# Kernel tuning notes

Measured on AMD Instinct MI355X. Metric: run time of the kernel, lower is better.

Reference implementation:

```python
import jax, jax.numpy as jnp
import numpy as np

DIM = 768
HEADS = 12


def setup_inputs() -> dict:
    key = jax.random.key(0)
    ks = jax.random.split(key, 7)
    B, N, S, C = 4, 1024, 1024, DIM
    query = jax.random.normal(ks[0], (B, N, C), dtype=jnp.float32)
    attn_weight = jax.random.normal(ks[1], (B, HEADS, N, S), dtype=jnp.float32) * 0.1
    s = 1.0 / np.sqrt(C)
    Wq = jax.random.normal(ks[2], (C, C), dtype=jnp.float32) * s
    Wk = jax.random.normal(ks[3], (C, C), dtype=jnp.float32) * s
    Wv = jax.random.normal(ks[4], (C, C), dtype=jnp.float32) * s
    Wo = jax.random.normal(ks[5], (C, C), dtype=jnp.float32) * s
    bo = jnp.zeros((C,), dtype=jnp.float32)
    return {"query": query, "attn_weight": attn_weight, "Wq": Wq, "Wk": Wk, "Wv": Wv, "Wo": Wo, "bo": bo}


def reference(query, attn_weight, Wq, Wk, Wv, Wo, bo):
    B, N, C = query.shape
    H = HEADS
    d = C // H
    scale = d ** -0.5
    # self-attention: key = value = query
    def heads(x):  # [B,N,C] -> [B,H,N,d]
        return x.reshape(B, -1, H, d).transpose(0, 2, 1, 3)
    q = heads(query @ Wq.T)
    k = heads(query @ Wk.T)
    v = heads(query @ Wv.T)
    attn = jnp.einsum('bhnd,bhsd->bhns', q, k) * scale
    log_attn = jax.nn.log_softmax(attn, axis=-1)
    attn = jax.nn.softmax(attn_weight + log_attn, axis=-1)
    out = jnp.einsum('bhns,bhsd->bhnd', attn, v)
    out = out.transpose(0, 2, 1, 3).reshape(B, N, C)
    out = out @ Wo.T + bo
    return out
```

## Files before the change

kernel.cpp:

```cpp
#include <hip/hip_runtime.h>
#include <cstdint>
#include <cstddef>

typedef unsigned short u16;
typedef unsigned int u32;
typedef float f32x4 __attribute__((ext_vector_type(4)));
typedef short bf16x8 __attribute__((ext_vector_type(8)));


#define GLOAD_LDS16(g, l)                                                        \
  __builtin_amdgcn_global_load_lds(                                              \
      (const __attribute__((address_space(1))) void*)(g),                        \
      (__attribute__((address_space(3))) void*)(l), 16, 0, 0)

__device__ __forceinline__ u16 f2bf(float f) {
  u32 u = __float_as_uint(f);
  u32 r = ((u >> 16) & 1u) + 0x7fffu;
  return (u16)((u + r) >> 16);
}

__device__ __forceinline__ float redmax16(float v) {
  v = fmaxf(v, __shfl_xor(v, 8, 16));
  v = fmaxf(v, __shfl_xor(v, 4, 16));
  v = fmaxf(v, __shfl_xor(v, 2, 16));
  v = fmaxf(v, __shfl_xor(v, 1, 16));
  return v;
}
__device__ __forceinline__ float redsum16(float v) {
  v += __shfl_xor(v, 8, 16);
  v += __shfl_xor(v, 4, 16);
  v += __shfl_xor(v, 2, 16);
  v += __shfl_xor(v, 1, 16);
  return v;
}

__global__ __launch_bounds__(256) void cast_all(
    const float* __restrict__ q, const float* __restrict__ wq, const float* __restrict__ wk,
    const float* __restrict__ wv, const float* __restrict__ wo,
    u16* __restrict__ X, u16* __restrict__ Wqkv, u16* __restrict__ Wob) {
  int id = blockIdx.x * 256 + threadIdx.x;
  const float* src;
  u16* dst;
  if (id < 786432) {
    src = q + (size_t)id * 4;       dst = X + (size_t)id * 4;
  } else if (id < 933888) {
    int o = id - 786432;  src = wq + (size_t)o * 4; dst = Wqkv + (size_t)o * 4;
  } else if (id < 1081344) {
    int o = id - 933888;  src = wk + (size_t)o * 4; dst = Wqkv + 589824 + (size_t)o * 4;
  } else if (id < 1228800) {
    int o = id - 1081344; src = wv + (size_t)o * 4; dst = Wqkv + 1179648 + (size_t)o * 4;
  } else {
    int o = id - 1228800; src = wo + (size_t)o * 4; dst = Wob + (size_t)o * 4;
  }
  float4 v = *(const float4*)src;
  uint2 o2;
  o2.x = (u32)f2bf(v.x) | ((u32)f2bf(v.y) << 16);
  o2.y = (u32)f2bf(v.z) | ((u32)f2bf(v.w) << 16);
  *(uint2*)dst = o2;
}

template <int MODE>
__global__ __launch_bounds__(256) void gemm_bt(
    const u16* __restrict__ A, const u16* __restrict__ Bm,
    u16* __restrict__ Cq, float* __restrict__ Cf, const float* __restrict__ bias) {
  constexpr int K = 768;
  __shared__ u16 As[128 * 64];
  __shared__ u16 Bs[128 * 64];
  const int tid = threadIdx.x;
  const int w = tid >> 6, lane = tid & 63, quad = lane >> 4, l16 = lane & 15;
  const int m0 = blockIdx.y * 128, n0 = blockIdx.x * 128;
  const int wm = (w >> 1) * 64, wn = (w & 1) * 64;
  const int xr = (l16 & 7) << 3;

  f32x4 acc[4][4];
#pragma unroll
  for (int i = 0; i < 4; ++i)
#pragma unroll
    for (int j = 0; j < 4; ++j)
#pragma unroll
      for (int r = 0; r < 4; ++r) acc[i][j][r] = 0.f;

  for (int kt = 0; kt < K; kt += 64) {
#pragma unroll
    for (int t = 0; t < 4; ++t) {
      int id = (t * 4 + w) * 64 + lane;
      int row = id >> 3;
      int scol = ((id & 7) ^ (row & 7)) << 3;
      GLOAD_LDS16(A + (size_t)(m0 + row) * K + kt + scol, As + (t * 4 + w) * 512);
      GLOAD_LDS16(Bm + (size_t)(n0 + row) * K + kt + scol, Bs + (t * 4 + w) * 512);
    }
    __syncthreads();
#pragma unroll
    for (int kk = 0; kk < 2; ++kk) {
      bf16x8 af[4], bfr[4];
#pragma unroll
      for (int mi = 0; mi < 4; ++mi)
        af[mi] = *(const bf16x8*)(As + (wm + mi * 16 + l16) * 64 + ((kk * 32 + quad * 8) ^ xr));
#pragma unroll
      for (int ni = 0; ni < 4; ++ni)
        bfr[ni] = *(const bf16x8*)(Bs + (wn + ni * 16 + l16) * 64 + ((kk * 32 + quad * 8) ^ xr));
#pragma unroll
      for (int mi = 0; mi < 4; ++mi)
#pragma unroll
        for (int ni = 0; ni < 4; ++ni)
          acc[mi][ni] = __builtin_amdgcn_mfma_f32_16x16x32_bf16(af[mi], bfr[ni], acc[mi][ni], 0, 0, 0);
    }
    __syncthreads();
  }

#pragma unroll
  for (int ni = 0; ni < 4; ++ni) {
    int cb = n0 + wn + ni * 16;
#pragma unroll
    for (int mi = 0; mi < 4; ++mi) {
#pragma unroll
      for (int r = 0; r < 4; ++r) {
        int m = m0 + wm + mi * 16 + quad * 4 + r;
        float v = acc[mi][ni][r];
        if (MODE == 0) {
          int t = cb / 768;
          int c = cb - t * 768;
          int h = c >> 6, dd = (c & 63) + l16;
          int b = m >> 10, ntok = m & 1023;
          Cq[(size_t)((t * 4 + b) * 12 + h) * 65536 + (size_t)ntok * 64 + dd] = f2bf(v);
        } else {
          int n = cb + l16;
          Cf[(size_t)m * 768 + n] = v + bias[n];
        }
      }
    }
  }
}

__global__ __launch_bounds__(256) void transpose_v(const u16* __restrict__ QKV,
                                                   u16* __restrict__ Vt) {
  __shared__ u16 tsm[64 * 72];
  const int bh = blockIdx.y, n0 = blockIdx.x * 64;
  const u16* V = QKV + (size_t)(96 + bh) * 65536;
  const int tid = threadIdx.x;
  const int r = tid >> 2, ch = tid & 3;
  *(int4*)(tsm + r * 72 + ch * 16) = *(const int4*)(V + (size_t)(n0 + r) * 64 + ch * 16);
  *(int4*)(tsm + r * 72 + ch * 16 + 8) = *(const int4*)(V + (size_t)(n0 + r) * 64 + ch * 16 + 8);
  __syncthreads();
  const int dd = tid >> 2;
  alignas(16) u16 buf[16];
#pragma unroll
  for (int i = 0; i < 16; ++i) buf[i] = tsm[(ch * 16 + i) * 72 + dd];
  u16* dst = Vt + ((size_t)bh * 64 + dd) * 1024 + n0 + ch * 16;
  *(int4*)dst = *(int4*)buf;
  *(int4*)(dst + 8) = *((int4*)buf + 1);
}

__global__ __launch_bounds__(256, 3) void attn_kernel(
    const u16* __restrict__ QKV, const u16* __restrict__ Vt,
    const float* __restrict__ W, u16* __restrict__ Oa) {
  __shared__ u16 Ks2[2][64 * 64];
  __shared__ u16 Vs2[2][64 * 64];
  __shared__ u16 Ps[4][16 * 72];
  const int tid = threadIdx.x;
  const int w = tid >> 6, lane = tid & 63, quad = lane >> 4, l16 = lane & 15;
  const int bh = blockIdx.y, q0 = blockIdx.x * 64;
  const u16* Qh = QKV + (size_t)bh * 65536;
  const u16* Kh = QKV + (size_t)(48 + bh) * 65536;
  const u16* Vth = Vt + (size_t)bh * 65536;
  const float* Wp = W + (size_t)bh * 1048576 + (size_t)(q0 + w * 16 + quad * 4) * 1024 + l16;
  const int xr = (l16 & 7) << 3;

  bf16x8 aq0, aq1;
  {
    int qrow = q0 + w * 16 + l16;
    aq0 = *(const bf16x8*)(Qh + (size_t)qrow * 64 + quad * 8);
    aq1 = *(const bf16x8*)(Qh + (size_t)qrow * 64 + 32 + quad * 8);
  }

  const int sid0 = (0 * 4 + w) * 64 + lane;
  const int sid1 = (1 * 4 + w) * 64 + lane;
  const int r0 = sid0 >> 3, sl0 = ((sid0 & 7) ^ (r0 & 7)) << 3;
  const int r1 = sid1 >> 3, sl1 = ((sid1 & 7) ^ (r1 & 7)) << 3;

  GLOAD_LDS16(Kh + (size_t)r0 * 64 + sl0, &Ks2[0][(0 * 4 + w) * 512]);
  GLOAD_LDS16(Kh + (size_t)r1 * 64 + sl1, &Ks2[0][(1 * 4 + w) * 512]);
  GLOAD_LDS16(Vth + (size_t)r0 * 1024 + sl0, &Vs2[0][(0 * 4 + w) * 512]);
  GLOAD_LDS16(Vth + (size_t)r1 * 1024 + sl1, &Vs2[0][(1 * 4 + w) * 512]);
  float wc[4][4];
#pragma unroll
  for (int r = 0; r < 4; ++r)
#pragma unroll
    for (int j = 0; j < 4; ++j) wc[j][r] = Wp[(size_t)r * 1024 + j * 16];

  f32x4 o[4];
  float mrow[4], lrow[4];
#pragma unroll
  for (int j = 0; j < 4; ++j)
#pragma unroll
    for (int r = 0; r < 4; ++r) o[j][r] = 0.f;
#pragma unroll
  for (int r = 0; r < 4; ++r) { mrow[r] = -1e30f; lrow[r] = 0.f; }

  for (int st = 0; st < 16; ++st) {
    const int cur = st & 1;
    __syncthreads();

    float wn[4][4];
    if (st < 15) {
      const int sn = (st + 1) * 64;
      GLOAD_LDS16(Kh + (size_t)(sn + r0) * 64 + sl0, &Ks2[cur ^ 1][(0 * 4 + w) * 512]);
      GLOAD_LDS16(Kh + (size_t)(sn + r1) * 64 + sl1, &Ks2[cur ^ 1][(1 * 4 + w) * 512]);
      GLOAD_LDS16(Vth + (size_t)r0 * 1024 + sn + sl0, &Vs2[cur ^ 1][(0 * 4 + w) * 512]);
      GLOAD_LDS16(Vth + (size_t)r1 * 1024 + sn + sl1, &Vs2[cur ^ 1][(1 * 4 + w) * 512]);
#pragma unroll
      for (int r = 0; r < 4; ++r)
#pragma unroll
        for (int j = 0; j < 4; ++j) wn[j][r] = Wp[(size_t)r * 1024 + sn + j * 16];
    }

    const u16* Kb = Ks2[cur];
    const u16* Vb = Vs2[cur];

    f32x4 sf[4];
#pragma unroll
    for (int j = 0; j < 4; ++j) {
#pragma unroll
      for (int r = 0; r < 4; ++r) sf[j][r] = 0.f;
      bf16x8 bk0 = *(const bf16x8*)(Kb + (j * 16 + l16) * 64 + ((quad * 8) ^ xr));
      bf16x8 bk1 = *(const bf16x8*)(Kb + (j * 16 + l16) * 64 + ((32 + quad * 8) ^ xr));
      sf[j] = __builtin_amdgcn_mfma_f32_16x16x32_bf16(aq0, bk0, sf[j], 0, 0, 0);
      sf[j] = __builtin_amdgcn_mfma_f32_16x16x32_bf16(aq1, bk1, sf[j], 0, 0, 0);
    }
    float lg[4][4];
#pragma unroll
    for (int j = 0; j < 4; ++j)
#pragma unroll
      for (int r = 0; r < 4; ++r) lg[j][r] = sf[j][r] * 0.125f + wc[j][r];

    float ps[4][4];
#pragma unroll
    for (int r = 0; r < 4; ++r) {
      float nm = fmaxf(fmaxf(lg[0][r], lg[1][r]), fmaxf(lg[2][r], lg[3][r]));
      nm = redmax16(nm);
      nm = fmaxf(nm, mrow[r]);
      float al = __expf(mrow[r] - nm);
      mrow[r] = nm;
      float rs = 0.f;
#pragma unroll
      for (int j = 0; j < 4; ++j) {
        ps[j][r] = __expf(lg[j][r] - nm);
        rs += ps[j][r];
      }
      rs = redsum16(rs);
      lrow[r] = lrow[r] * al + rs;
#pragma unroll
      for (int jd = 0; jd < 4; ++jd) o[jd][r] *= al;
    }
    u16* Pw = Ps[w];
#pragma unroll
    for (int j = 0; j < 4; ++j)
#pragma unroll
      for (int r = 0; r < 4; ++r) Pw[(quad * 4 + r) * 72 + j * 16 + l16] = f2bf(ps[j][r]);
#pragma unroll
    for (int kk = 0; kk < 2; ++kk) {
      bf16x8 ap = *(const bf16x8*)(Pw + l16 * 72 + kk * 32 + quad * 8);
#pragma unroll
      for (int jd = 0; jd < 4; ++jd) {
        bf16x8 bv = *(const bf16x8*)(Vb + (jd * 16 + l16) * 64 + ((kk * 32 + quad * 8) ^ xr));
        o[jd] = __builtin_amdgcn_mfma_f32_16x16x32_bf16(ap, bv, o[jd], 0, 0, 0);
      }
    }
    if (st < 15) {
#pragma unroll
      for (int r = 0; r < 4; ++r)
#pragma unroll
        for (int j = 0; j < 4; ++j) wc[j][r] = wn[j][r];
    }
  }

  const int b = bh / 12, h = bh - (bh / 12) * 12;
#pragma unroll
  for (int jd = 0; jd < 4; ++jd)
#pragma unroll
    for (int r = 0; r < 4; ++r) {
      int row = b * 1024 + q0 + w * 16 + quad * 4 + r;
      int col = h * 64 + jd * 16 + l16;
      Oa[(size_t)row * 768 + col] = f2bf(o[jd][r] / lrow[r]);
    }
}

extern "C" void kernel_launch(void* const* d_in, const int* in_sizes, int n_in,
                              void* d_out, int out_size, void* d_ws, size_t ws_size,
                              hipStream_t stream) {
  const float* q  = (const float*)d_in[0];
  const float* aw = (const float*)d_in[1];
  const float* wq = (const float*)d_in[2];
  const float* wk = (const float*)d_in[3];
  const float* wv = (const float*)d_in[4];
  const float* wo = (const float*)d_in[5];
  const float* bo = (const float*)d_in[6];
  float* out = (float*)d_out;
  char* ws = (char*)d_ws;
  u16* X    = (u16*)(ws);
  u16* Wqkv = (u16*)(ws + 6291456);
  u16* Wob  = (u16*)(ws + 9830400);
  u16* QKV  = (u16*)(ws + 11010048);
  u16* Vt   = (u16*)(ws + 29884416);
  u16* Oa   = (u16*)(ws + 36175872);

  cast_all<<<5376, 256, 0, stream>>>(q, wq, wk, wv, wo, X, Wqkv, Wob);
  gemm_bt<0><<<dim3(18, 32), 256, 0, stream>>>(X, Wqkv, QKV, nullptr, nullptr);
  transpose_v<<<dim3(16, 48), 256, 0, stream>>>(QKV, Vt);
  attn_kernel<<<dim3(16, 48), 256, 0, stream>>>(QKV, Vt, aw, Oa);
  gemm_bt<1><<<dim3(6, 32), 256, 0, stream>>>(Oa, Wob, nullptr, out, bo);
}
```

Baseline: 369.7 us.

## Add 64-row output GEMM, raise attention occupancy, swizzle P buffer

Replaces the output projection GEMM with a 64x128-tile variant, launching twice as many blocks so more CUs stay busy on the small 4096x768 problem. The attention kernel's launch bound goes from 3 to 4 blocks per CU. Its P scratch buffer switches from padded rows to an XOR-swizzled 64-wide layout, which shrinks LDS use and avoids bank conflicts. The final normalization uses a reciprocal multiply instead of a division. The tighter register budget could cause spills, and the smaller GEMM tile reuses each loaded operand less.

```diff
diff --git a/kernel.cpp b/kernel.cpp
--- a/kernel.cpp
+++ b/kernel.cpp
@@ -132,6 +132,69 @@
   }
 }
 
+__global__ __launch_bounds__(256) void gemm_bt64(
+    const u16* __restrict__ A, const u16* __restrict__ Bm,
+    float* __restrict__ Cf, const float* __restrict__ bias) {
+  constexpr int K = 768;
+  __shared__ u16 As[64 * 64];
+  __shared__ u16 Bs[128 * 64];
+  const int tid = threadIdx.x;
+  const int w = tid >> 6, lane = tid & 63, quad = lane >> 4, l16 = lane & 15;
+  const int m0 = blockIdx.y * 64, n0 = blockIdx.x * 128;
+  const int wm = (w >> 1) * 32, wn = (w & 1) * 64;
+  const int xr = (l16 & 7) << 3;
+
+  f32x4 acc[2][4];
+#pragma unroll
+  for (int i = 0; i < 2; ++i)
+#pragma unroll
+    for (int j = 0; j < 4; ++j)
+#pragma unroll
+      for (int r = 0; r < 4; ++r) acc[i][j][r] = 0.f;
+
+  for (int kt = 0; kt < K; kt += 64) {
+#pragma unroll
+    for (int t = 0; t < 4; ++t) {
+      int id = (t * 4 + w) * 64 + lane;
+      int row = id >> 3, scol = ((id & 7) ^ (row & 7)) << 3;
+      GLOAD_LDS16(Bm + (size_t)(n0 + row) * K + kt + scol, Bs + (t * 4 + w) * 512);
+      if (t < 2) {
+        GLOAD_LDS16(A + (size_t)(m0 + row) * K + kt + scol, As + (t * 4 + w) * 512);
+      }
+    }
+    __syncthreads();
+#pragma unroll
+    for (int kk = 0; kk < 2; ++kk) {
+      bf16x8 af[2], bfr[4];
+#pragma unroll
+      for (int mi = 0; mi < 2; ++mi)
+        af[mi] = *(const bf16x8*)(As + (wm + mi * 16 + l16) * 64 + ((kk * 32 + quad * 8) ^ xr));
+#pragma unroll
+      for (int ni = 0; ni < 4; ++ni)
+        bfr[ni] = *(const bf16x8*)(Bs + (wn + ni * 16 + l16) * 64 + ((kk * 32 + quad * 8) ^ xr));
+#pragma unroll
+      for (int mi = 0; mi < 2; ++mi)
+#pragma unroll
+        for (int ni = 0; ni < 4; ++ni)
+          acc[mi][ni] = __builtin_amdgcn_mfma_f32_16x16x32_bf16(af[mi], bfr[ni], acc[mi][ni], 0, 0, 0);
+    }
+    __syncthreads();
+  }
+
+#pragma unroll
+  for (int ni = 0; ni < 4; ++ni) {
+    int n = n0 + wn + ni * 16 + l16;
+#pragma unroll
+    for (int mi = 0; mi < 2; ++mi) {
+#pragma unroll
+      for (int r = 0; r < 4; ++r) {
+        int m = m0 + wm + mi * 16 + quad * 4 + r;
+        Cf[(size_t)m * 768 + n] = acc[mi][ni][r] + bias[n];
+      }
+    }
+  }
+}
+
 __global__ __launch_bounds__(256) void transpose_v(const u16* __restrict__ QKV,
                                                    u16* __restrict__ Vt) {
   __shared__ u16 tsm[64 * 72];
@@ -151,12 +214,12 @@
   *(int4*)(dst + 8) = *((int4*)buf + 1);
 }
 
-__global__ __launch_bounds__(256, 3) void attn_kernel(
+__global__ __launch_bounds__(256, 4) void attn_kernel(
     const u16* __restrict__ QKV, const u16* __restrict__ Vt,
     const float* __restrict__ W, u16* __restrict__ Oa) {
   __shared__ u16 Ks2[2][64 * 64];
   __shared__ u16 Vs2[2][64 * 64];
-  __shared__ u16 Ps[4][16 * 72];
+  __shared__ u16 Ps[4][16 * 64];
   const int tid = threadIdx.x;
   const int w = tid >> 6, lane = tid & 63, quad = lane >> 4, l16 = lane & 15;
   const int bh = blockIdx.y, q0 = blockIdx.x * 64;
@@ -256,10 +319,13 @@
 #pragma unroll
     for (int j = 0; j < 4; ++j)
 #pragma unroll
-      for (int r = 0; r < 4; ++r) Pw[(quad * 4 + r) * 72 + j * 16 + l16] = f2bf(ps[j][r]);
+      for (int r = 0; r < 4; ++r) {
+        int prow = quad * 4 + r;
+        Pw[prow * 64 + ((j * 16 + l16) ^ ((prow & 7) << 3))] = f2bf(ps[j][r]);
+      }
 #pragma unroll
     for (int kk = 0; kk < 2; ++kk) {
-      bf16x8 ap = *(const bf16x8*)(Pw + l16 * 72 + kk * 32 + quad * 8);
+      bf16x8 ap = *(const bf16x8*)(Pw + l16 * 64 + ((kk * 32 + quad * 8) ^ xr));
 #pragma unroll
       for (int jd = 0; jd < 4; ++jd) {
         bf16x8 bv = *(const bf16x8*)(Vb + (jd * 16 + l16) * 64 + ((kk * 32 + quad * 8) ^ xr));
@@ -275,13 +341,16 @@
   }
 
   const int b = bh / 12, h = bh - (bh / 12) * 12;
+  float il[4];
+#pragma unroll
+  for (int r = 0; r < 4; ++r) il[r] = __builtin_amdgcn_rcpf(lrow[r]);
 #pragma unroll
   for (int jd = 0; jd < 4; ++jd)
 #pragma unroll
     for (int r = 0; r < 4; ++r) {
       int row = b * 1024 + q0 + w * 16 + quad * 4 + r;
       int col = h * 64 + jd * 16 + l16;
-      Oa[(size_t)row * 768 + col] = f2bf(o[jd][r] / lrow[r]);
+      Oa[(size_t)row * 768 + col] = f2bf(o[jd][r] * il[r]);
     }
 }
 
@@ -308,5 +377,5 @@
   gemm_bt<0><<<dim3(18, 32), 256, 0, stream>>>(X, Wqkv, QKV, nullptr, nullptr);
   transpose_v<<<dim3(16, 48), 256, 0, stream>>>(QKV, Vt);
   attn_kernel<<<dim3(16, 48), 256, 0, stream>>>(QKV, Vt, aw, Oa);
-  gemm_bt<1><<<dim3(6, 32), 256, 0, stream>>>(Oa, Wob, nullptr, out, bo);
-}
+  gemm_bt64<<<dim3(6, 64), 256, 0, stream>>>(Oa, Wob, out, bo);
+}
```

After: 370.1 us. About the same (+0.1%).
